# Optimization experiments

Measured on AMD Instinct MI355X. Metric: run time of the kernel, lower is better.

Reference implementation:

```python
import jax, jax.numpy as jnp
import numpy as np

HEADS = 12
EMBED = 768
HEAD_DIM = EMBED // HEADS


def setup_inputs() -> dict:
    key = jax.random.key(0)
    kx, kw, kb = jax.random.split(key, 3)
    x = jax.random.normal(kx, (8, 1024, EMBED), dtype=jnp.float32)
    # nn.Linear(embed, 3*embed): weight (3E, E), bias (3E,)
    W_qkv = jax.random.normal(kw, (3 * EMBED, EMBED), dtype=jnp.float32) * (1.0 / np.sqrt(EMBED))
    b_qkv = jax.random.normal(kb, (3 * EMBED,), dtype=jnp.float32) * 0.01
    return {"x": x, "W_qkv": W_qkv, "b_qkv": b_qkv}


def reference(x, W_qkv, b_qkv):
    b, n, e = x.shape
    qkv = x @ W_qkv.T + b_qkv                       # (b, n, 3E)
    qkv = qkv.reshape(b, n, HEADS, 3 * HEAD_DIM)    # (b, n, h, 3d)
    q, k, v = jnp.split(qkv, 3, axis=-1)            # each (b, n, h, d)
    scores = jnp.einsum('bihd,bjhd->bijh', q, k) / np.sqrt(HEAD_DIM)
    attn = jax.nn.softmax(scores, axis=-2)          # softmax over keys j (dim=-2)
    out = jnp.einsum('bijh,bjhd->bihd', attn, v)
    return out.reshape(b, n, e)
```

## Files before the change

kernel.cpp:

```cpp
#include <hip/hip_runtime.h>
#include <hip/hip_bf16.h>
#include <cstdint>

#define BATCH 8
#define SEQ   1024
#define EMB   768
#define HEADS 12
#define HDIM  64
#define C3    2304
#define MROWS (BATCH*SEQ)
#define KSLC  (EMB / 16)

typedef __attribute__((ext_vector_type(8)))  short bf16x8;
typedef __attribute__((ext_vector_type(4)))  short bf16x4;
typedef __attribute__((ext_vector_type(4)))  float f32x4;
typedef __attribute__((ext_vector_type(16))) float f32x16;

static __device__ inline short f2bf(float f) {
    union { float f; uint32_t u; } v; v.f = f;
    uint32_t u = v.u + 0x7fff + ((v.u >> 16) & 1);
    return (short)(u >> 16);
}

__global__ __launch_bounds__(256) void pack_bf16(const float* __restrict__ in,
                                                 short* __restrict__ out) {
    const int tid = blockIdx.x * 256 + threadIdx.x;
    const int r    = tid & 31;
    const int ks   = (tid >> 5) % KSLC;
    const int tile = tid / (KSLC * 32);
    const int row  = tile * 32 + r;

    const float* src = in + (size_t)row * EMB + ks * 16;
    float4 v0 = ((const float4*)src)[0];
    float4 v1 = ((const float4*)src)[1];
    float4 v2 = ((const float4*)src)[2];
    float4 v3 = ((const float4*)src)[3];
    bf16x8 o0 = { f2bf(v0.x), f2bf(v0.y), f2bf(v0.z), f2bf(v0.w),
                  f2bf(v1.x), f2bf(v1.y), f2bf(v1.z), f2bf(v1.w) };
    bf16x8 o1 = { f2bf(v2.x), f2bf(v2.y), f2bf(v2.z), f2bf(v2.w),
                  f2bf(v3.x), f2bf(v3.y), f2bf(v3.z), f2bf(v3.w) };
    short* dst = out + (size_t)tid * 16;
    *(bf16x8*)(dst)     = o0;
    *(bf16x8*)(dst + 8) = o1;
}

__global__ __launch_bounds__(256) void qkv_gemm_mfma(const short* __restrict__ xb2,
                                                     const short* __restrict__ Wb2,
                                                     const float* __restrict__ bias,
                                                     short* __restrict__ qkvb) {
    const int bx = blockIdx.x;
    const int by = blockIdx.y;
    const int t = threadIdx.x;
    const int w = t >> 6;
    const int lane = t & 63;
    const int l5  = lane >> 5;
    const int r31 = lane & 31;
    const int m0 = by * 128, n0 = bx * 128;
    const int wm = (w & 1) * 64, wn = (w >> 1) * 64;

    const int laneoff = r31 * 16 + l5 * 8;
    const short* pa0 = xb2 + ((size_t)((m0 + wm) >> 5) * KSLC) * 512 + laneoff;
    const short* pa1 = pa0 + (size_t)KSLC * 512;
    const short* pb0 = Wb2 + ((size_t)((n0 + wn) >> 5) * KSLC) * 512 + laneoff;
    const short* pb1 = pb0 + (size_t)KSLC * 512;

    f32x16 acc[2][2] = {};

    #pragma unroll 4
    for (int ks = 0; ks < KSLC; ++ks) {
        bf16x8 a0 = *(const bf16x8*)(pa0 + ks * 512);
        bf16x8 a1 = *(const bf16x8*)(pa1 + ks * 512);
        bf16x8 b0 = *(const bf16x8*)(pb0 + ks * 512);
        bf16x8 b1 = *(const bf16x8*)(pb1 + ks * 512);
        acc[0][0] = __builtin_amdgcn_mfma_f32_32x32x16_bf16(a0, b0, acc[0][0], 0, 0, 0);
        acc[0][1] = __builtin_amdgcn_mfma_f32_32x32x16_bf16(a0, b1, acc[0][1], 0, 0, 0);
        acc[1][0] = __builtin_amdgcn_mfma_f32_32x32x16_bf16(a1, b0, acc[1][0], 0, 0, 0);
        acc[1][1] = __builtin_amdgcn_mfma_f32_32x32x16_bf16(a1, b1, acc[1][1], 0, 0, 0);
    }

    float bsv[2], scl[2];
    #pragma unroll
    for (int nt = 0; nt < 2; ++nt) {
        int n = n0 + wn + nt * 32 + r31;
        bsv[nt] = bias[n];
        scl[nt] = ((n % 192) < 64) ? 0.125f : 1.0f;
    }
    #pragma unroll
    for (int mt = 0; mt < 2; ++mt)
        #pragma unroll
        for (int nt = 0; nt < 2; ++nt) {
            int n = n0 + wn + nt * 32 + r31;
            #pragma unroll
            for (int reg = 0; reg < 16; ++reg) {
                int row = (reg & 3) + 8 * (reg >> 2) + 4 * l5;
                int m = m0 + wm + mt * 32 + row;
                float v = (acc[mt][nt][reg] + bsv[nt]) * scl[nt];
                qkvb[(size_t)m * C3 + n] = f2bf(v);
            }
        }
}

__global__ __launch_bounds__(256) void v_transpose(const short* __restrict__ qkvb,
                                                   short* __restrict__ vt) {
    __shared__ int Lt[64][65];

    const int bh = blockIdx.x;
    const int jt = blockIdx.y;
    const int b = bh / HEADS, h = bh % HEADS;
    const int t = threadIdx.x;
    const int j0 = jt * 64;
    const size_t base = (size_t)b * SEQ * C3 + (size_t)h * 192 + 128;

    #pragma unroll
    for (int p = 0; p < 2; ++p) {
        int idx = p * 256 + t;
        int j = idx >> 3, d0 = (idx & 7) * 8;
        bf16x8 v = *(const bf16x8*)(qkvb + base + (size_t)(j0 + j) * C3 + d0);
        #pragma unroll
        for (int u = 0; u < 8; ++u)
            Lt[d0 + u][j] = (int)(unsigned short)v[u];
    }
    __syncthreads();
    #pragma unroll
    for (int p = 0; p < 2; ++p) {
        int idx = p * 256 + t;
        int d = idx >> 3, c8 = (idx & 7) * 8;
        bf16x8 o;
        #pragma unroll
        for (int u = 0; u < 8; ++u)
            o[u] = (short)Lt[d][c8 + u];
        *(bf16x8*)(vt + ((size_t)bh * 64 + d) * SEQ + j0 + c8) = o;
    }
}

#define LDP 72

__global__ __launch_bounds__(256, 4) void attn_mfma(const short* __restrict__ qkvb,
                                                    const short* __restrict__ vt,
                                                    float* __restrict__ out) {
    __shared__ short Ks[64][LDP];
    __shared__ short Vt[64][LDP];
    __shared__ short Ps[64][LDP];

    const int bx   = blockIdx.x;
    const int qt   = bx & 15;
    const int h    = (bx >> 4) % HEADS;
    const int b    = bx / (16 * HEADS);
    const int t    = threadIdx.x;
    const int w    = t >> 6;
    const int lane = t & 63;
    const int c    = lane & 15;
    const int q    = lane >> 4;
    const int i0   = qt * 64;

    const size_t base = (size_t)b * SEQ * C3 + (size_t)h * 192;
    const short* vtb = vt + (size_t)(b * HEADS + h) * 64 * SEQ;

    #pragma unroll
    for (int p = 0; p < 2; ++p) {
        int idx = p * 256 + t;
        int i = idx >> 3, d0 = (idx & 7) << 3;
        *(bf16x8*)&Ps[i][d0] =
            *(const bf16x8*)(qkvb + base + (size_t)(i0 + i) * C3 + d0);
    }
    __syncthreads();
    const bf16x8 aq0 = *(bf16x8*)&Ps[w * 16 + c][q * 8];
    const bf16x8 aq1 = *(bf16x8*)&Ps[w * 16 + c][32 + q * 8];

    f32x4 o[4] = {{0.f,0.f,0.f,0.f},{0.f,0.f,0.f,0.f},
                  {0.f,0.f,0.f,0.f},{0.f,0.f,0.f,0.f}};
    float l_acc = 0.f;

    for (int kt = 0; kt < 16; ++kt) {
        const int j0 = kt * 64;
        __syncthreads();
        #pragma unroll
        for (int p = 0; p < 2; ++p) {
            int idx = p * 256 + t;
            int j = idx >> 3, d0 = (idx & 7) << 3;
            *(bf16x8*)&Ks[j][d0] =
                *(const bf16x8*)(qkvb + base + 64 + (size_t)(j0 + j) * C3 + d0);
        }
        #pragma unroll
        for (int p = 0; p < 2; ++p) {
            int idx = p * 256 + t;
            int d = idx >> 3, j8 = (idx & 7) << 3;
            *(bf16x8*)&Vt[d][j8] =
                *(const bf16x8*)(vtb + (size_t)d * SEQ + j0 + j8);
        }
        __syncthreads();

        f32x4 s[4];
        #pragma unroll
        for (int mt = 0; mt < 4; ++mt) {
            bf16x8 a0 = *(bf16x8*)&Ks[mt * 16 + c][q * 8];
            bf16x8 a1 = *(bf16x8*)&Ks[mt * 16 + c][32 + q * 8];
            f32x4 acc = {0.f, 0.f, 0.f, 0.f};
            acc = __builtin_amdgcn_mfma_f32_16x16x32_bf16(a0, aq0, acc, 0, 0, 0);
            acc = __builtin_amdgcn_mfma_f32_16x16x32_bf16(a1, aq1, acc, 0, 0, 0);
            s[mt] = acc;
        }

        #pragma unroll
        for (int mt = 0; mt < 4; ++mt) {
            float p0 = __expf(s[mt][0]);
            float p1 = __expf(s[mt][1]);
            float p2 = __expf(s[mt][2]);
            float p3 = __expf(s[mt][3]);
            l_acc += (p0 + p1) + (p2 + p3);
            bf16x4 pw = { f2bf(p0), f2bf(p1), f2bf(p2), f2bf(p3) };
            *(bf16x4*)&Ps[w * 16 + c][mt * 16 + 4 * q] = pw;
        }

        bf16x8 ap0 = *(bf16x8*)&Ps[w * 16 + c][q * 8];
        bf16x8 ap1 = *(bf16x8*)&Ps[w * 16 + c][32 + q * 8];
        #pragma unroll
        for (int dt = 0; dt < 4; ++dt) {
            bf16x8 b0 = *(bf16x8*)&Vt[dt * 16 + c][q * 8];
            bf16x8 b1 = *(bf16x8*)&Vt[dt * 16 + c][32 + q * 8];
            o[dt] = __builtin_amdgcn_mfma_f32_16x16x32_bf16(ap0, b0, o[dt], 0, 0, 0);
            o[dt] = __builtin_amdgcn_mfma_f32_16x16x32_bf16(ap1, b1, o[dt], 0, 0, 0);
        }
    }

    l_acc += __shfl_xor(l_acc, 16, 64);
    l_acc += __shfl_xor(l_acc, 32, 64);
    float linv[4];
    #pragma unroll
    for (int r = 0; r < 4; ++r)
        linv[r] = 1.0f / __shfl(l_acc, 4 * q + r, 64);

    #pragma unroll
    for (int dt = 0; dt < 4; ++dt)
        #pragma unroll
        for (int r = 0; r < 4; ++r) {
            int i = w * 16 + q * 4 + r;
            out[((size_t)b * SEQ + i0 + i) * EMB + h * HDIM + dt * 16 + c]
                = o[dt][r] * linv[r];
        }
}

extern "C" void kernel_launch(void* const* d_in, const int* in_sizes, int n_in,
                              void* d_out, int out_size, void* d_ws, size_t ws_size,
                              hipStream_t stream) {
    const float* x    = (const float*)d_in[0];
    const float* W    = (const float*)d_in[1];
    const float* bias = (const float*)d_in[2];
    float* out = (float*)d_out;

    short* xb2  = (short*)d_ws;
    short* Wb2  = xb2 + (size_t)MROWS * EMB;
    short* qkvb = Wb2 + (size_t)C3 * EMB;
    short* vt   = qkvb + (size_t)MROWS * C3;

    pack_bf16<<<MROWS * KSLC / 256, 256, 0, stream>>>(x, xb2);
    pack_bf16<<<C3 * KSLC / 256, 256, 0, stream>>>(W, Wb2);

    dim3 g1(C3 / 128, MROWS / 128);
    qkv_gemm_mfma<<<g1, 256, 0, stream>>>(xb2, Wb2, bias, qkvb);

    dim3 g2(BATCH * HEADS, SEQ / 64);
    v_transpose<<<g2, 256, 0, stream>>>(qkvb, vt);

    attn_mfma<<<BATCH * HEADS * (SEQ / 64), 256, 0, stream>>>(qkvb, vt, out);
}
```

Baseline: 181.9 us.

## Process 128 query rows per attention block to reuse K/V tiles

Doubles the query tile per attention block from 64 to 128 rows, with each wave computing two 16-row subtiles against the same K and V tiles loaded into shared memory. This halves K/V global loads and LDS staging per query row and amortizes K/V register fragments across two MFMA chains. In exchange it raises register and LDS use (occupancy hint lowered to 3 blocks per CU) and halves the number of blocks launched.

After: 182.0 us. About the same (+0.0%).

```diff
diff --git a/kernel.cpp b/kernel.cpp
--- a/kernel.cpp
+++ b/kernel.cpp
@@ -135,41 +135,44 @@
 
 #define LDP 72
 
-__global__ __launch_bounds__(256, 4) void attn_mfma(const short* __restrict__ qkvb,
+__global__ __launch_bounds__(256, 3) void attn_mfma(const short* __restrict__ qkvb,
                                                     const short* __restrict__ vt,
                                                     float* __restrict__ out) {
     __shared__ short Ks[64][LDP];
     __shared__ short Vt[64][LDP];
-    __shared__ short Ps[64][LDP];
+    __shared__ short Ps[128][LDP];
 
     const int bx   = blockIdx.x;
-    const int qt   = bx & 15;
-    const int h    = (bx >> 4) % HEADS;
-    const int b    = bx / (16 * HEADS);
+    const int qt   = bx & 7;
+    const int h    = (bx >> 3) % HEADS;
+    const int b    = bx / (8 * HEADS);
     const int t    = threadIdx.x;
     const int w    = t >> 6;
     const int lane = t & 63;
     const int c    = lane & 15;
     const int q    = lane >> 4;
-    const int i0   = qt * 64;
+    const int i0   = qt * 128;
 
     const size_t base = (size_t)b * SEQ * C3 + (size_t)h * 192;
     const short* vtb = vt + (size_t)(b * HEADS + h) * 64 * SEQ;
 
     #pragma unroll
-    for (int p = 0; p < 2; ++p) {
+    for (int p = 0; p < 4; ++p) {
         int idx = p * 256 + t;
         int i = idx >> 3, d0 = (idx & 7) << 3;
         *(bf16x8*)&Ps[i][d0] =
             *(const bf16x8*)(qkvb + base + (size_t)(i0 + i) * C3 + d0);
     }
     __syncthreads();
-    const bf16x8 aq0 = *(bf16x8*)&Ps[w * 16 + c][q * 8];
-    const bf16x8 aq1 = *(bf16x8*)&Ps[w * 16 + c][32 + q * 8];
-
-    f32x4 o[4] = {{0.f,0.f,0.f,0.f},{0.f,0.f,0.f,0.f},
-                  {0.f,0.f,0.f,0.f},{0.f,0.f,0.f,0.f}};
-    float l_acc = 0.f;
+    bf16x8 aq[2][2];
+    #pragma unroll
+    for (int s = 0; s < 2; ++s) {
+        aq[s][0] = *(bf16x8*)&Ps[w * 32 + s * 16 + c][q * 8];
+        aq[s][1] = *(bf16x8*)&Ps[w * 32 + s * 16 + c][32 + q * 8];
+    }
+
+    f32x4 o[2][4] = {};
+    float l_acc[2] = {0.f, 0.f};
 
     for (int kt = 0; kt < 16; ++kt) {
         const int j0 = kt * 64;
@@ -190,54 +193,77 @@
         }
         __syncthreads();
 
-        f32x4 s[4];
+        bf16x8 ka[4][2];
         #pragma unroll
         for (int mt = 0; mt < 4; ++mt) {
-            bf16x8 a0 = *(bf16x8*)&Ks[mt * 16 + c][q * 8];
-            bf16x8 a1 = *(bf16x8*)&Ks[mt * 16 + c][32 + q * 8];
-            f32x4 acc = {0.f, 0.f, 0.f, 0.f};
-            acc = __builtin_amdgcn_mfma_f32_16x16x32_bf16(a0, aq0, acc, 0, 0, 0);
-            acc = __builtin_amdgcn_mfma_f32_16x16x32_bf16(a1, aq1, acc, 0, 0, 0);
-            s[mt] = acc;
-        }
-
-        #pragma unroll
-        for (int mt = 0; mt < 4; ++mt) {
-            float p0 = __expf(s[mt][0]);
-            float p1 = __expf(s[mt][1]);
-            float p2 = __expf(s[mt][2]);
-            float p3 = __expf(s[mt][3]);
-            l_acc += (p0 + p1) + (p2 + p3);
-            bf16x4 pw = { f2bf(p0), f2bf(p1), f2bf(p2), f2bf(p3) };
-            *(bf16x4*)&Ps[w * 16 + c][mt * 16 + 4 * q] = pw;
-        }
-
-        bf16x8 ap0 = *(bf16x8*)&Ps[w * 16 + c][q * 8];
-        bf16x8 ap1 = *(bf16x8*)&Ps[w * 16 + c][32 + q * 8];
+            ka[mt][0] = *(bf16x8*)&Ks[mt * 16 + c][q * 8];
+            ka[mt][1] = *(bf16x8*)&Ks[mt * 16 + c][32 + q * 8];
+        }
+
+        f32x4 s[2][4];
+        #pragma unroll
+        for (int ss = 0; ss < 2; ++ss)
+            #pragma unroll
+            for (int mt = 0; mt < 4; ++mt) {
+                f32x4 acc = {0.f, 0.f, 0.f, 0.f};
+                acc = __builtin_amdgcn_mfma_f32_16x16x32_bf16(ka[mt][0], aq[ss][0], acc, 0, 0, 0);
+                acc = __builtin_amdgcn_mfma_f32_16x16x32_bf16(ka[mt][1], aq[ss][1], acc, 0, 0, 0);
+                s[ss][mt] = acc;
+            }
+
+        #pragma unroll
+        for (int ss = 0; ss < 2; ++ss)
+            #pragma unroll
+            for (int mt = 0; mt < 4; ++mt) {
+                float p0 = __expf(s[ss][mt][0]);
+                float p1 = __expf(s[ss][mt][1]);
+                float p2 = __expf(s[ss][mt][2]);
+                float p3 = __expf(s[ss][mt][3]);
+                l_acc[ss] += (p0 + p1) + (p2 + p3);
+                bf16x4 pw = { f2bf(p0), f2bf(p1), f2bf(p2), f2bf(p3) };
+                *(bf16x4*)&Ps[w * 32 + ss * 16 + c][mt * 16 + 4 * q] = pw;
+            }
+
+        bf16x8 vb[4][2];
         #pragma unroll
         for (int dt = 0; dt < 4; ++dt) {
-            bf16x8 b0 = *(bf16x8*)&Vt[dt * 16 + c][q * 8];
-            bf16x8 b1 = *(bf16x8*)&Vt[dt * 16 + c][32 + q * 8];
-            o[dt] = __builtin_amdgcn_mfma_f32_16x16x32_bf16(ap0, b0, o[dt], 0, 0, 0);
-            o[dt] = __builtin_amdgcn_mfma_f32_16x16x32_bf16(ap1, b1, o[dt], 0, 0, 0);
-        }
-    }
-
-    l_acc += __shfl_xor(l_acc, 16, 64);
-    l_acc += __shfl_xor(l_acc, 32, 64);
-    float linv[4];
-    #pragma unroll
-    for (int r = 0; r < 4; ++r)
-        linv[r] = 1.0f / __shfl(l_acc, 4 * q + r, 64);
-
-    #pragma unroll
-    for (int dt = 0; dt < 4; ++dt)
-        #pragma unroll
-        for (int r = 0; r < 4; ++r) {
-            int i = w * 16 + q * 4 + r;
-            out[((size_t)b * SEQ + i0 + i) * EMB + h * HDIM + dt * 16 + c]
-                = o[dt][r] * linv[r];
-        }
+            vb[dt][0] = *(bf16x8*)&Vt[dt * 16 + c][q * 8];
+            vb[dt][1] = *(bf16x8*)&Vt[dt * 16 + c][32 + q * 8];
+        }
+
+        #pragma unroll
+        for (int ss = 0; ss < 2; ++ss) {
+            bf16x8 ap0 = *(bf16x8*)&Ps[w * 32 + ss * 16 + c][q * 8];
+            bf16x8 ap1 = *(bf16x8*)&Ps[w * 32 + ss * 16 + c][32 + q * 8];
+            #pragma unroll
+            for (int dt = 0; dt < 4; ++dt) {
+                o[ss][dt] = __builtin_amdgcn_mfma_f32_16x16x32_bf16(ap0, vb[dt][0], o[ss][dt], 0, 0, 0);
+                o[ss][dt] = __builtin_amdgcn_mfma_f32_16x16x32_bf16(ap1, vb[dt][1], o[ss][dt], 0, 0, 0);
+            }
+        }
+    }
+
+    float linv[2][4];
+    #pragma unroll
+    for (int ss = 0; ss < 2; ++ss) {
+        float v = l_acc[ss];
+        v += __shfl_xor(v, 16, 64);
+        v += __shfl_xor(v, 32, 64);
+        #pragma unroll
+        for (int r = 0; r < 4; ++r)
+            linv[ss][r] = 1.0f / __shfl(v, 4 * q + r, 64);
+    }
+
+    #pragma unroll
+    for (int ss = 0; ss < 2; ++ss)
+        #pragma unroll
+        for (int dt = 0; dt < 4; ++dt)
+            #pragma unroll
+            for (int r = 0; r < 4; ++r) {
+                int i = w * 32 + ss * 16 + q * 4 + r;
+                out[((size_t)b * SEQ + i0 + i) * EMB + h * HDIM + dt * 16 + c]
+                    = o[ss][dt][r] * linv[ss][r];
+            }
 }
 
 extern "C" void kernel_launch(void* const* d_in, const int* in_sizes, int n_in,
@@ -262,5 +288,5 @@
     dim3 g2(BATCH * HEADS, SEQ / 64);
     v_transpose<<<g2, 256, 0, stream>>>(qkvb, vt);
 
-    attn_mfma<<<BATCH * HEADS * (SEQ / 64), 256, 0, stream>>>(qkvb, vt, out);
-}
+    attn_mfma<<<BATCH * HEADS * (SEQ / 128), 256, 0, stream>>>(qkvb, vt, out);
+}
```
